# Performance work log

Hardware: AMD Instinct MI355X
Metric: run time of the kernel (lower is better)

Reference implementation:

```python
import jax, jax.numpy as jnp
import numpy as np

B, S, D_IN, D_Q, D_V, H = 2, 2048, 1024, 1024, 1024, 16
HD_Q, HD_V = D_Q // H, D_V // H
SCALE = float(D_Q) ** 0.5  # source scales by sqrt(d_q), NOT sqrt(head_dim)


def setup_inputs() -> dict:
    key = jax.random.key(0)
    k1, k2, k3, k4, k5 = jax.random.split(key, 5)
    return {
        "x": jax.random.normal(k1, (B, S, D_IN), dtype=jnp.float32),
        "w_q": jax.random.normal(k2, (D_IN, D_Q), dtype=jnp.float32),
        "w_k": jax.random.normal(k3, (D_IN, D_Q), dtype=jnp.float32),
        "w_v": jax.random.normal(k4, (D_IN, D_V), dtype=jnp.float32),
        "W_o": jax.random.normal(k5, (D_IN, D_V), dtype=jnp.float32),
    }


def reference(x, w_q, w_k, w_v, W_o):
    b, s, _ = x.shape
    # projections: [b, s, d]
    q = x @ w_q
    k = x @ w_k
    v = x @ w_v
    # split heads -> [b, h, s, hd]
    Q = q.reshape(b, s, H, HD_Q).transpose(0, 2, 1, 3)
    K = k.reshape(b, s, H, HD_Q).transpose(0, 2, 1, 3)
    V = v.reshape(b, s, H, HD_V).transpose(0, 2, 1, 3)
    # full [b, h, s, s] score matrix (naive attention, as in source)
    scores = jnp.einsum("bhqd,bhkd->bhqk", Q, K)
    # FAITHFUL QUIRK: source applies softmax over dim=0 (batch axis)
    attn = jax.nn.softmax(scores / SCALE, axis=0)
    vals = jnp.einsum("bhqk,bhkd->bhqd", attn, V)
    vals = vals.transpose(0, 2, 1, 3).reshape(b, s, D_V)
    return vals @ W_o
```

## Files before the change

kernel.cpp:

```cpp
#include <hip/hip_runtime.h>


typedef _Float16 f16;
typedef __attribute__((ext_vector_type(8))) _Float16 f16x8;
typedef __attribute__((ext_vector_type(4))) _Float16 f16x4;
typedef __attribute__((ext_vector_type(4))) float f32x4;
typedef __attribute__((ext_vector_type(16))) float f32x16;

#define MFMA16(a,b,c)  __builtin_amdgcn_mfma_f32_16x16x32_f16(a,b,c,0,0,0)
#define MFMA32(a,b,c)  __builtin_amdgcn_mfma_f32_32x32x16_f16(a,b,c,0,0,0)
#define GLD16(gp, lp) __builtin_amdgcn_global_load_lds(                         \
    (const __attribute__((address_space(1))) void*)(gp),                        \
    (__attribute__((address_space(3))) void*)(lp), 16, 0, 0)

__global__ __launch_bounds__(256) void prep(const float* __restrict__ x,
                                            const float* __restrict__ w0, const float* __restrict__ w1,
                                            const float* __restrict__ w2, const float* __restrict__ w3,
                                            f16* __restrict__ xh,
                                            f16* __restrict__ o0, f16* __restrict__ o1,
                                            f16* __restrict__ o2, f16* __restrict__ o3) {
    const int bb = blockIdx.x;
    const int tid = threadIdx.x;
    if (bb >= 1024) {
        int i = (bb - 1024) * 256 + tid;
        float4 v = ((const float4*)x)[i];
        f16x4 h;
        h[0] = (f16)v.x; h[1] = (f16)v.y; h[2] = (f16)v.z; h[3] = (f16)v.w;
        *(f16x4*)(xh + (long)i * 4) = h;
        return;
    }
    const float* w; f16* o;
    switch (bb & 3) {
        case 0: w = w0; o = o0; break;
        case 1: w = w1; o = o1; break;
        case 2: w = w2; o = o2; break;
        default: w = w3; o = o3; break;
    }
    __shared__ alignas(16) f16 t[64][72];
    const int d0 = ((bb >> 2) & 15) * 64, j0 = (bb >> 6) * 64;
    #pragma unroll
    for (int it = 0; it < 4; ++it) {
        int idx = it * 256 + tid;
        int row = idx >> 4, c4 = idx & 15;
        float4 v = *(const float4*)(w + (long)(d0 + row) * 1024 + j0 + c4 * 4);
        f16x4 h;
        h[0] = (f16)v.x; h[1] = (f16)v.y; h[2] = (f16)v.z; h[3] = (f16)v.w;
        *(f16x4*)&t[row][c4 * 4] = h;
    }
    __syncthreads();
    #pragma unroll
    for (int it = 0; it < 4; ++it) {
        int idx = it * 256 + tid;
        int jr = idx >> 4, d4 = idx & 15;
        f16x4 h;
        #pragma unroll
        for (int m = 0; m < 4; ++m) h[m] = t[d4 * 4 + m][jr];
        *(f16x4*)(o + (long)(j0 + jr) * 1024 + d0 + d4 * 4) = h;
    }
}

__global__ __launch_bounds__(256, 1) void gemm_qkv(const f16* __restrict__ A,
                                                   const f16* __restrict__ Wt,
                                                   f16* __restrict__ Qc,
                                                   f16* __restrict__ Kc,
                                                   f16* __restrict__ Vtg) {
    __shared__ alignas(16) f16 smem[16384];
    f16* As = smem;
    f16* Bs = smem + 8192;
    const int tid = threadIdx.x;
    const int wave = tid >> 6, lane = tid & 63;
    const int l15 = lane & 15, lq = lane >> 4;
    const int sw = l15 & 7;
    const int m0 = blockIdx.x * 128, n0 = blockIdx.y * 128;
    const int wr = (wave >> 1) * 64, wc = (wave & 1) * 64;
    const int r8 = lane >> 3;
    const int swc8 = ((lane & 7) ^ r8) * 8;

    f32x4 acc[4][4] = {};

    for (int kt = 0; kt < 16; ++kt) {
        __syncthreads();
        #pragma unroll
        for (int i = 0; i < 4; ++i) {
            GLD16(A  + (long)(m0 + wave * 32 + i * 8 + r8) * 1024 + kt * 64 + swc8, As + (wave * 32 + i * 8) * 64);
            GLD16(Wt + (long)(n0 + wave * 32 + i * 8 + r8) * 1024 + kt * 64 + swc8, Bs + (wave * 32 + i * 8) * 64);
        }
        __syncthreads();
        #pragma unroll
        for (int s2 = 0; s2 < 2; ++s2) {
            const int rc = ((s2 * 4 + lq) ^ sw) << 3;
            f16x8 af[4], bf[4];
            #pragma unroll
            for (int i = 0; i < 4; ++i) af[i] = *(const f16x8*)&As[(wr + i * 16 + l15) * 64 + rc];
            #pragma unroll
            for (int j = 0; j < 4; ++j) bf[j] = *(const f16x8*)&Bs[(wc + j * 16 + l15) * 64 + rc];
            #pragma unroll
            for (int i = 0; i < 4; ++i)
                #pragma unroll
                for (int j = 0; j < 4; ++j)
                    acc[i][j] = MFMA16(af[i], bf[j], acc[i][j]);
        }
    }

    const int sel = n0 >> 10;
    const int nb = n0 - (sel << 10);

    if (sel < 2) {
        f16* dst = sel == 0 ? Qc : Kc;
        const int b = m0 >> 11;
        const int boff = b ? 0 : 64;
        const float qs = sel == 0 ? 0.045084219f
                                  : (b == 0 ? -1.0f : 1.0f);
        __syncthreads();
        #pragma unroll
        for (int i = 0; i < 4; ++i)
            #pragma unroll
            for (int j = 0; j < 4; ++j) {
                int row0 = wr + i * 16 + lq * 4;
                int colb = wc + j * 16 + l15;
                int chunk = colb >> 3, sub = colb & 7;
                #pragma unroll
                for (int r = 0; r < 4; ++r) {
                    int row = row0 + r;
                    smem[row * 128 + ((chunk ^ (row & 7)) << 3) + sub] = (f16)(acc[i][j][r] * qs);
                }
            }
        __syncthreads();
        #pragma unroll
        for (int e = 0; e < 8; ++e) {
            int id = e * 256 + tid;
            int row = id >> 4, c = id & 15;
            f16x8 v = *(const f16x8*)&smem[row * 128 + ((c ^ (row & 7)) << 3)];
            int gr = m0 + row, s = gr & 2047;
            int gc = nb + c * 8, hh = gc >> 6, hd = gc & 63;
            *(f16x8*)(dst + (long)(hh * 2048 + s) * 128 + boff + hd) = v;
        }
    } else {
        #pragma unroll
        for (int i = 0; i < 4; ++i)
            #pragma unroll
            for (int j = 0; j < 4; ++j) {
                int gr0 = m0 + wr + i * 16 + lq * 4;
                int gc  = nb + wc + j * 16 + l15;
                int b = gr0 >> 11, s = gr0 & 2047;
                int hh = gc >> 6, hd = gc & 63;
                f16x4 v;
                #pragma unroll
                for (int r = 0; r < 4; ++r) v[r] = (f16)acc[i][j][r];
                *(f16x4*)(Vtg + (long)((b * 16 + hh) * 64 + hd) * 2048 + s) = v;
            }
    }
}

template<int NSUM>
__global__ __launch_bounds__(256, 1) void gemm_out(const f16* __restrict__ A0,
                                                   const f16* __restrict__ A1,
                                                   const f16* __restrict__ A2,
                                                   const f16* __restrict__ A3,
                                                   const f16* __restrict__ Bt,
                                                   float* __restrict__ outp) {
    __shared__ alignas(16) f16 As[64][72];
    __shared__ alignas(16) f16 Bs[128][64];
    const int tid = threadIdx.x;
    const int wave = tid >> 6, lane = tid & 63;
    const int l15 = lane & 15, lq = lane >> 4;
    const int sw = l15 & 7;
    const int m0 = blockIdx.x * 64, n0 = blockIdx.y * 128;
    const int wr = (wave >> 1) * 32, wc = (wave & 1) * 64;
    const int r8 = lane >> 3;
    const int swc8 = ((lane & 7) ^ r8) * 8;

    f32x4 acc[2][4] = {};

    for (int kt = 0; kt < 16; ++kt) {
        __syncthreads();
        #pragma unroll
        for (int it = 0; it < 2; ++it) {
            int idx = it * 256 + tid;
            int row = idx >> 3, c = idx & 7;
            long off = (long)(m0 + row) * 1024 + kt * 64 + c * 8;
            f16x8 a = *(const f16x8*)(A0 + off) + *(const f16x8*)(A1 + off);
            if constexpr (NSUM >= 3) a = a + *(const f16x8*)(A2 + off);
            if constexpr (NSUM >= 4) a = a + *(const f16x8*)(A3 + off);
            *(f16x8*)&As[row][c * 8] = a;
        }
        #pragma unroll
        for (int i = 0; i < 4; ++i)
            GLD16(Bt + (long)(n0 + wave * 32 + i * 8 + r8) * 1024 + kt * 64 + swc8, &Bs[wave * 32 + i * 8][0]);
        __syncthreads();
        #pragma unroll
        for (int s2 = 0; s2 < 2; ++s2) {
            const int rc = ((s2 * 4 + lq) ^ sw) << 3;
            f16x8 af[2], bf[4];
            #pragma unroll
            for (int i = 0; i < 2; ++i) af[i] = *(const f16x8*)&As[wr + i * 16 + l15][s2 * 32 + lq * 8];
            #pragma unroll
            for (int j = 0; j < 4; ++j) bf[j] = *(const f16x8*)&Bs[wc + j * 16 + l15][rc];
            #pragma unroll
            for (int i = 0; i < 2; ++i)
                #pragma unroll
                for (int j = 0; j < 4; ++j)
                    acc[i][j] = MFMA16(af[i], bf[j], acc[i][j]);
        }
    }

    #pragma unroll
    for (int i = 0; i < 2; ++i)
        #pragma unroll
        for (int j = 0; j < 4; ++j) {
            int gr0 = m0 + wr + i * 16 + lq * 4;
            int gc  = n0 + wc + j * 16 + l15;
            #pragma unroll
            for (int r = 0; r < 4; ++r)
                outp[(long)(gr0 + r) * 1024 + gc] = acc[i][j][r];
        }
}

__global__ __launch_bounds__(256, 2) void attention_kernel(const f16* __restrict__ Qc,
                                                           const f16* __restrict__ Kc,
                                                           const f16* __restrict__ Vtg,
                                                           f16* __restrict__ v0,
                                                           f16* __restrict__ v1,
                                                           f16* __restrict__ v2,
                                                           f16* __restrict__ v3) {
    __shared__ alignas(16) f16 KsC[3][32][128];
    __shared__ alignas(16) f16 Vts[3][2][64][32];
    const int tid = threadIdx.x;
    const int wave = tid >> 6, lane = tid & 63;
    const int l31 = lane & 31, hi = lane >> 5;
    const int kch = l31 & 15;
    const int vcb = (l31 >> 1) & 3;

    const int bid = blockIdx.x;
    const int xcd = bid & 7, sl = bid >> 3;
    const int h  = xcd * 2 + (sl & 1);
    const int qt = (sl >> 1) & 7, ks = sl >> 4;
    const int q0 = qt * 256;
    const int key0 = ks * 512;
    const int nt = 16;
    f16* vals = ks == 0 ? v0 : ks == 1 ? v1 : ks == 2 ? v2 : v3;
    const int qr = q0 + wave * 64;

    f16x8 qfr[2][8];
    #pragma unroll
    for (int g = 0; g < 2; ++g)
        #pragma unroll
        for (int s2 = 0; s2 < 8; ++s2)
            qfr[g][s2] = *(const f16x8*)(Qc + (long)(h * 2048 + qr + g * 32 + l31) * 128
                                         + s2 * 16 + hi * 8);

    f32x16 acc[2][2][2] = {};

    const int kw = wave & 1;
    const f16* kbase = Kc + (long)(h * 2048 + key0 + kw * 16 + (lane >> 4)) * 128;
    const int tb = wave & 1;
    const f16* vbase = Vtg + (long)((tb * 16 + h) * 64 + (lane >> 2)) * 2048 + key0
                       + ((lane & 3) ^ ((lane >> 3) & 3)) * 8;

    auto stage = [&](int kt, int buf) {
        if (wave < 2) {
            f16* l = &KsC[buf][0][0] + kw * 2048;
            #pragma unroll
            for (int i = 0; i < 4; ++i) {
                const int gch = ((lane & 15) ^ ((i << 2) | (lane >> 4))) << 3;
                GLD16(kbase + (long)kt * 4096 + i * 512 + gch, l + i * 512);
            }
        } else {
            const f16* g = vbase + kt * 32;
            f16* l = &Vts[buf][tb][0][0];
            #pragma unroll
            for (int i = 0; i < 4; ++i) GLD16(g + (long)i * 16 * 2048, l + i * 512);
        }
    };

    const f16* VtsF = &Vts[0][0][0][0];
    const f16x8 ones8 = {(f16)1.f,(f16)1.f,(f16)1.f,(f16)1.f,(f16)1.f,(f16)1.f,(f16)1.f,(f16)1.f};

    stage(0, 0);
    stage(1, 1);
    int cur = 0, nx2 = 2;
    for (int kt = 0; kt < nt; ++kt) {
        if (kt == nt - 1) asm volatile("s_waitcnt vmcnt(0)" ::: "memory");
        else              asm volatile("s_waitcnt vmcnt(4)" ::: "memory");
        __builtin_amdgcn_s_barrier();
        __builtin_amdgcn_sched_barrier(0);
        if (kt + 2 < nt) stage(kt + 2, nx2);

        f16x8 pf0[2][2];
        #pragma unroll
        for (int g = 0; g < 2; ++g) {
            f32x16 S = {};
            __builtin_amdgcn_s_setprio(1);
            #pragma unroll
            for (int s2 = 0; s2 < 8; ++s2) {
                f16x8 a = *(const f16x8*)&KsC[cur][l31][(((s2 * 2 + hi) ^ kch) << 3)];
                S = MFMA32(a, qfr[g][s2], S);
            }
            __builtin_amdgcn_s_setprio(0);

            unsigned pk[8];
            #pragma unroll
            for (int p = 0; p < 8; ++p) {
                float e0 = __builtin_amdgcn_exp2f(S[2 * p]);
                float e1 = __builtin_amdgcn_exp2f(S[2 * p + 1]);
                float pa = __builtin_amdgcn_rcpf(1.0f + e0);
                float pb = __builtin_amdgcn_rcpf(1.0f + e1);
                auto h2 = __builtin_amdgcn_cvt_pkrtz(pa, pb);
                pk[p] = __builtin_bit_cast(unsigned, h2);
            }
            #pragma unroll
            for (int keyh = 0; keyh < 2; ++keyh) {
                unsigned a0 = pk[4 * keyh + 0], b0 = pk[4 * keyh + 2];
                unsigned a1 = pk[4 * keyh + 1], b1 = pk[4 * keyh + 3];
                asm("v_permlane32_swap_b32 %0, %1" : "+v"(a0), "+v"(b0));
                asm("v_permlane32_swap_b32 %0, %1" : "+v"(a1), "+v"(b1));
                union { unsigned u[4]; f16x8 v; } m;
                m.u[0] = a0; m.u[1] = a1; m.u[2] = b0; m.u[3] = b1;
                pf0[g][keyh] = m.v;
            }
        }

        __builtin_amdgcn_s_setprio(1);
        #pragma unroll
        for (int pb = 0; pb < 2; ++pb)
            #pragma unroll
            for (int keyh = 0; keyh < 2; ++keyh) {
                f16x8 vf[2];
                #pragma unroll
                for (int hdh = 0; hdh < 2; ++hdh)
                    vf[hdh] = *(const f16x8*)&VtsF[cur * 4096 + pb * 2048 + hdh * 1024
                                                   + l31 * 32 + (((keyh * 2 + hi) ^ vcb) << 3)];
                #pragma unroll
                for (int g = 0; g < 2; ++g) {
                    const f16x8 pfr = pb ? (ones8 - pf0[g][keyh]) : pf0[g][keyh];
                    #pragma unroll
                    for (int hdh = 0; hdh < 2; ++hdh)
                        acc[pb][g][hdh] = MFMA32(vf[hdh], pfr, acc[pb][g][hdh]);
                }
            }
        __builtin_amdgcn_s_setprio(0);

        cur = cur == 2 ? 0 : cur + 1;
        nx2 = nx2 == 2 ? 0 : nx2 + 1;
    }

    #pragma unroll
    for (int pb = 0; pb < 2; ++pb)
        #pragma unroll
        for (int g = 0; g < 2; ++g)
            #pragma unroll
            for (int hdh = 0; hdh < 2; ++hdh)
                #pragma unroll
                for (int gg = 0; gg < 4; ++gg) {
                    f16x4 ov;
                    #pragma unroll
                    for (int r2 = 0; r2 < 4; ++r2) ov[r2] = (f16)acc[pb][g][hdh][gg * 4 + r2];
                    *(f16x4*)(vals + (long)(pb * 2048 + qr + g * 32 + l31) * 1024
                              + h * 64 + hdh * 32 + gg * 8 + hi * 4) = ov;
                }
}

extern "C" void kernel_launch(void* const* d_in, const int* in_sizes, int n_in,
                              void* d_out, int out_size, void* d_ws, size_t ws_size,
                              hipStream_t stream) {
    const float* x  = (const float*)d_in[0];
    const float* wq = (const float*)d_in[1];
    const float* wk = (const float*)d_in[2];
    const float* wv = (const float*)d_in[3];
    const float* wo = (const float*)d_in[4];

    char* ws = (char*)d_ws;
    f16* xh    = (f16*)(ws);
    f16* wqT   = (f16*)(ws + 8388608);
    f16* wkT   = (f16*)(ws + 10485760);
    f16* wvT   = (f16*)(ws + 12582912);
    f16* woT   = (f16*)(ws + 14680064);
    f16* Qc    = (f16*)(ws + 16777216);
    f16* Kc    = (f16*)(ws + 25165824);
    f16* Vtg   = (f16*)(ws + 33554432);
    f16* vals1 = (f16*)(ws + 41943040);
    f16* vals2 = (f16*)(ws + 50331648);
    f16* vals3 = (f16*)(ws + 58720256);
    f16* vals0 = xh;
    (void)in_sizes; (void)n_in; (void)out_size; (void)ws_size;

    prep<<<5120, 256, 0, stream>>>(x, wq, wk, wv, wo, xh, wqT, wkT, wvT, woT);

    gemm_qkv<<<dim3(32, 24), 256, 0, stream>>>(xh, wqT, Qc, Kc, Vtg);

    attention_kernel<<<512, 256, 0, stream>>>(Qc, Kc, Vtg, vals0, vals1, vals2, vals3);

    gemm_out<4><<<dim3(64, 8), 256, 0, stream>>>(vals0, vals1, vals2, vals3, woT, (float*)d_out);
}
```

Measured before the change: 191.3 us.

## Double-buffer 64-key attention tiles instead of triple-buffered 32-key tiles

Moves the attention kernel from a 3-stage pipeline over 32-key tiles to a 2-stage double buffer over 64-key tiles, halving the number of barrier iterations. Each tile is split into two 32-key halves, and both query groups share each K fragment load in the score MFMAs. The V tile layout and swizzle change to 64 keys wide. The wait now drains all loads (vmcnt(0)) every iteration, which cuts prefetch depth and may expose more load latency.

```diff
diff --git a/kernel.cpp b/kernel.cpp
--- a/kernel.cpp
+++ b/kernel.cpp
@@ -223,13 +223,13 @@
                                                            f16* __restrict__ v1,
                                                            f16* __restrict__ v2,
                                                            f16* __restrict__ v3) {
-    __shared__ alignas(16) f16 KsC[3][32][128];
-    __shared__ alignas(16) f16 Vts[3][2][64][32];
+    __shared__ alignas(16) f16 KsC[2][64][128];
+    __shared__ alignas(16) f16 Vts[2][2][64][64];
     const int tid = threadIdx.x;
     const int wave = tid >> 6, lane = tid & 63;
     const int l31 = lane & 31, hi = lane >> 5;
     const int kch = l31 & 15;
-    const int vcb = (l31 >> 1) & 3;
+    const int vch = l31 & 7;
 
     const int bid = blockIdx.x;
     const int xcd = bid & 7, sl = bid >> 3;
@@ -237,7 +237,7 @@
     const int qt = (sl >> 1) & 7, ks = sl >> 4;
     const int q0 = qt * 256;
     const int key0 = ks * 512;
-    const int nt = 16;
+    const int nt = 8;
     f16* vals = ks == 0 ? v0 : ks == 1 ? v1 : ks == 2 ? v2 : v3;
     const int qr = q0 + wave * 64;
 
@@ -252,96 +252,95 @@
     f32x16 acc[2][2][2] = {};
 
     const int kw = wave & 1;
-    const f16* kbase = Kc + (long)(h * 2048 + key0 + kw * 16 + (lane >> 4)) * 128;
+    const f16* kbase = Kc + (long)(h * 2048 + key0 + kw * 32 + (lane >> 4)) * 128;
     const int tb = wave & 1;
-    const f16* vbase = Vtg + (long)((tb * 16 + h) * 64 + (lane >> 2)) * 2048 + key0
-                       + ((lane & 3) ^ ((lane >> 3) & 3)) * 8;
+    const f16* vbase = Vtg + (long)((tb * 16 + h) * 64 + (lane >> 3)) * 2048 + key0
+                       + ((lane & 7) ^ ((lane >> 3) & 7)) * 8;
 
     auto stage = [&](int kt, int buf) {
         if (wave < 2) {
-            f16* l = &KsC[buf][0][0] + kw * 2048;
-            #pragma unroll
-            for (int i = 0; i < 4; ++i) {
-                const int gch = ((lane & 15) ^ ((i << 2) | (lane >> 4))) << 3;
-                GLD16(kbase + (long)kt * 4096 + i * 512 + gch, l + i * 512);
+            f16* l = &KsC[buf][kw * 32][0];
+            #pragma unroll
+            for (int i = 0; i < 8; ++i) {
+                const int gch = ((lane & 15) ^ (((i & 3) << 2) | (lane >> 4))) << 3;
+                GLD16(kbase + (long)kt * 8192 + i * 512 + gch, l + i * 512);
             }
         } else {
-            const f16* g = vbase + kt * 32;
+            const f16* g = vbase + kt * 64;
             f16* l = &Vts[buf][tb][0][0];
             #pragma unroll
-            for (int i = 0; i < 4; ++i) GLD16(g + (long)i * 16 * 2048, l + i * 512);
+            for (int i = 0; i < 8; ++i) GLD16(g + (long)i * 8 * 2048, l + i * 512);
         }
     };
 
-    const f16* VtsF = &Vts[0][0][0][0];
     const f16x8 ones8 = {(f16)1.f,(f16)1.f,(f16)1.f,(f16)1.f,(f16)1.f,(f16)1.f,(f16)1.f,(f16)1.f};
 
     stage(0, 0);
-    stage(1, 1);
-    int cur = 0, nx2 = 2;
     for (int kt = 0; kt < nt; ++kt) {
-        if (kt == nt - 1) asm volatile("s_waitcnt vmcnt(0)" ::: "memory");
-        else              asm volatile("s_waitcnt vmcnt(4)" ::: "memory");
+        const int cur = kt & 1;
+        asm volatile("s_waitcnt vmcnt(0)" ::: "memory");
         __builtin_amdgcn_s_barrier();
         __builtin_amdgcn_sched_barrier(0);
-        if (kt + 2 < nt) stage(kt + 2, nx2);
-
-        f16x8 pf0[2][2];
-        #pragma unroll
-        for (int g = 0; g < 2; ++g) {
-            f32x16 S = {};
+        if (kt + 1 < nt) stage(kt + 1, cur ^ 1);
+
+        #pragma unroll
+        for (int hkey = 0; hkey < 2; ++hkey) {
+            f32x16 S0 = {}, S1 = {};
             __builtin_amdgcn_s_setprio(1);
             #pragma unroll
             for (int s2 = 0; s2 < 8; ++s2) {
-                f16x8 a = *(const f16x8*)&KsC[cur][l31][(((s2 * 2 + hi) ^ kch) << 3)];
-                S = MFMA32(a, qfr[g][s2], S);
+                f16x8 a = *(const f16x8*)&KsC[cur][hkey * 32 + l31][(((s2 * 2 + hi) ^ kch) << 3)];
+                S0 = MFMA32(a, qfr[0][s2], S0);
+                S1 = MFMA32(a, qfr[1][s2], S1);
             }
             __builtin_amdgcn_s_setprio(0);
 
-            unsigned pk[8];
-            #pragma unroll
-            for (int p = 0; p < 8; ++p) {
-                float e0 = __builtin_amdgcn_exp2f(S[2 * p]);
-                float e1 = __builtin_amdgcn_exp2f(S[2 * p + 1]);
-                float pa = __builtin_amdgcn_rcpf(1.0f + e0);
-                float pb = __builtin_amdgcn_rcpf(1.0f + e1);
-                auto h2 = __builtin_amdgcn_cvt_pkrtz(pa, pb);
-                pk[p] = __builtin_bit_cast(unsigned, h2);
-            }
-            #pragma unroll
-            for (int keyh = 0; keyh < 2; ++keyh) {
-                unsigned a0 = pk[4 * keyh + 0], b0 = pk[4 * keyh + 2];
-                unsigned a1 = pk[4 * keyh + 1], b1 = pk[4 * keyh + 3];
-                asm("v_permlane32_swap_b32 %0, %1" : "+v"(a0), "+v"(b0));
-                asm("v_permlane32_swap_b32 %0, %1" : "+v"(a1), "+v"(b1));
-                union { unsigned u[4]; f16x8 v; } m;
-                m.u[0] = a0; m.u[1] = a1; m.u[2] = b0; m.u[3] = b1;
-                pf0[g][keyh] = m.v;
-            }
-        }
-
-        __builtin_amdgcn_s_setprio(1);
-        #pragma unroll
-        for (int pb = 0; pb < 2; ++pb)
-            #pragma unroll
-            for (int keyh = 0; keyh < 2; ++keyh) {
-                f16x8 vf[2];
-                #pragma unroll
-                for (int hdh = 0; hdh < 2; ++hdh)
-                    vf[hdh] = *(const f16x8*)&VtsF[cur * 4096 + pb * 2048 + hdh * 1024
-                                                   + l31 * 32 + (((keyh * 2 + hi) ^ vcb) << 3)];
-                #pragma unroll
-                for (int g = 0; g < 2; ++g) {
-                    const f16x8 pfr = pb ? (ones8 - pf0[g][keyh]) : pf0[g][keyh];
+            f16x8 pf0[2][2];
+            #pragma unroll
+            for (int g = 0; g < 2; ++g) {
+                const f32x16& S = g ? S1 : S0;
+                unsigned pk[8];
+                #pragma unroll
+                for (int p = 0; p < 8; ++p) {
+                    float e0 = __builtin_amdgcn_exp2f(S[2 * p]);
+                    float e1 = __builtin_amdgcn_exp2f(S[2 * p + 1]);
+                    float pa = __builtin_amdgcn_rcpf(1.0f + e0);
+                    float pb = __builtin_amdgcn_rcpf(1.0f + e1);
+                    auto h2 = __builtin_amdgcn_cvt_pkrtz(pa, pb);
+                    pk[p] = __builtin_bit_cast(unsigned, h2);
+                }
+                #pragma unroll
+                for (int keyh = 0; keyh < 2; ++keyh) {
+                    unsigned a0 = pk[4 * keyh + 0], b0 = pk[4 * keyh + 2];
+                    unsigned a1 = pk[4 * keyh + 1], b1 = pk[4 * keyh + 3];
+                    asm("v_permlane32_swap_b32 %0, %1" : "+v"(a0), "+v"(b0));
+                    asm("v_permlane32_swap_b32 %0, %1" : "+v"(a1), "+v"(b1));
+                    union { unsigned u[4]; f16x8 v; } m;
+                    m.u[0] = a0; m.u[1] = a1; m.u[2] = b0; m.u[3] = b1;
+                    pf0[g][keyh] = m.v;
+                }
+            }
+
+            __builtin_amdgcn_s_setprio(1);
+            #pragma unroll
+            for (int pb = 0; pb < 2; ++pb)
+                #pragma unroll
+                for (int keyh = 0; keyh < 2; ++keyh) {
+                    f16x8 vf[2];
                     #pragma unroll
                     for (int hdh = 0; hdh < 2; ++hdh)
-                        acc[pb][g][hdh] = MFMA32(vf[hdh], pfr, acc[pb][g][hdh]);
-                }
-            }
-        __builtin_amdgcn_s_setprio(0);
-
-        cur = cur == 2 ? 0 : cur + 1;
-        nx2 = nx2 == 2 ? 0 : nx2 + 1;
+                        vf[hdh] = *(const f16x8*)&Vts[cur][pb][hdh * 32 + l31]
+                                      [(((hkey * 4 + keyh * 2 + hi) ^ vch) << 3)];
+                    #pragma unroll
+                    for (int g = 0; g < 2; ++g) {
+                        const f16x8 pfr = pb ? (ones8 - pf0[g][keyh]) : pf0[g][keyh];
+                        #pragma unroll
+                        for (int hdh = 0; hdh < 2; ++hdh)
+                            acc[pb][g][hdh] = MFMA32(vf[hdh], pfr, acc[pb][g][hdh]);
+                    }
+                }
+            __builtin_amdgcn_s_setprio(0);
+        }
     }
 
     #pragma unroll
```

After: 202.7 us. 6.0% more time.
